# Kernel optimization log

Measured on AMD Instinct MI355X. Metric: run time of the kernel, lower is better.

Reference implementation:

```python
import jax, jax.numpy as jnp
import numpy as np

T1, T2, T3 = 0.05, 0.1, 0.15
EPS = 1e-8  # matches torch cosine_similarity clamp


def _propagate(x, t):
    # GEmbedding: cosine-similarity adjacency  [B,N,F] -> [B,N,N]
    xn = x / jnp.maximum(jnp.linalg.norm(x, axis=-1, keepdims=True), EPS)
    adj = jnp.einsum('bnf,bmf->bnm', xn, xn)
    # F.threshold(adj, t, 0): keep values strictly greater than t
    adj = jnp.where(adj > t, adj, 0.0)
    # GraphAdjNorm: D^{-1/2} A D^{-1/2} via row/col broadcast (same math as
    # the original diag-matmul, without materializing diagonal matrices)
    d = jnp.sum(adj, axis=-1)              # [B,N]
    inv_sqrt = 1.0 / jnp.sqrt(d)           # [B,N]
    adj = adj * inv_sqrt[..., :, None] * inv_sqrt[..., None, :]
    return jnp.einsum('bnm,bmf->bnf', adj, x)


def setup_inputs() -> dict:
    key = jax.random.key(0)
    k1, k2 = jax.random.split(key)
    B, N, F = 8, 2048, 128
    x = jax.random.normal(k1, (B, N, F), dtype=jnp.float32)
    weight = jax.random.normal(k2, (F, F), dtype=jnp.float32) * 0.05
    return {"x": x, "weight": weight}


def reference(x, weight):
    res = x
    h = x
    for t in (T1, T2, T3):
        h = _propagate(h, t)
    h = jax.lax.stop_gradient(h)  # torch.no_grad() block
    return jnp.einsum('bnf,fo->bno', h + res, weight)
```

## Files before the change

kernel.cpp:

```cpp
#include <hip/hip_runtime.h>
#include <hip/hip_bf16.h>
#include <cstdint>

#define BQ 8
#define NQ 2048
#define FQ 128
#define NG (NQ * 16)
#define HSS 256.0f

typedef __attribute__((ext_vector_type(8))) short short8;
typedef __attribute__((ext_vector_type(4))) float f32x4;
typedef __attribute__((ext_vector_type(8))) unsigned short us8;
typedef __attribute__((ext_vector_type(2))) unsigned int u32x2;
typedef __attribute__((ext_vector_type(4))) unsigned int u32x4;

__device__ __forceinline__ unsigned short f2bf(float f) {
    union { float f; unsigned int u; } c; c.f = f;
    unsigned int u = c.u;
    u = (u + 0x7FFFu + ((u >> 16) & 1u)) >> 16;
    return (unsigned short)u;
}
__device__ __forceinline__ float bf2f(unsigned short u) {
    union { unsigned int i; float f; } c; c.i = (unsigned int)u << 16; return c.f;
}
__device__ __forceinline__ unsigned int pk8lo(float a, float b, unsigned int old) {
    return (unsigned int)__builtin_amdgcn_cvt_pk_fp8_f32(a, b, (int)old, false);
}
__device__ __forceinline__ unsigned int pk8hi(float a, float b, unsigned int old) {
    return (unsigned int)__builtin_amdgcn_cvt_pk_fp8_f32(a, b, (int)old, true);
}


__global__ __launch_bounds__(256) void k_rownorm(const float* __restrict__ h,
                                                 unsigned short* __restrict__ xnF,
                                                 const float* __restrict__ W,
                                                 unsigned short* __restrict__ WF) {
    int t = threadIdx.x;
    if (blockIdx.x < 8) {
        int b = blockIdx.x;
        int c2 = t & 15, fc = t >> 4;
        us8 u;
        #pragma unroll
        for (int e = 0; e < 8; ++e)
            u[e] = f2bf(W[(size_t)(fc * 8 + e) * FQ + b * 16 + c2]);
        *(us8*)(WF + b * 2048 + fc * 128 + c2 * 8) = u;
        return;
    }
    int bid = blockIdx.x - 8;
    int rl = t >> 4, j = t & 15;
    size_t row = (size_t)bid * 16 + rl;
    const float* hr = h + row * FQ + j * 8;
    float v[8];
    #pragma unroll
    for (int e = 0; e < 8; ++e) v[e] = hr[e];
    float s = 0.f;
    #pragma unroll
    for (int e = 0; e < 8; ++e) s += v[e] * v[e];
    s += __shfl_xor(s, 1, 64);
    s += __shfl_xor(s, 2, 64);
    s += __shfl_xor(s, 4, 64);
    s += __shfl_xor(s, 8, 64);
    float inv = 1.0f / fmaxf(sqrtf(s), 1e-8f);
    us8 u;
    #pragma unroll
    for (int e = 0; e < 8; ++e) u[e] = f2bf(v[e] * inv);
    *(us8*)(xnF + (size_t)bid * 2048 + j * 128 + rl * 8) = u;
}

__global__ __launch_bounds__(512) void k_adj(const unsigned short* __restrict__ xnF,
                                             unsigned char* __restrict__ adjF,
                                             float* __restrict__ dpart, float t) {
    __shared__ unsigned short As[16384];
    __shared__ union { unsigned short Bsh[16384];
                       unsigned char  T2[128 * 132]; } ub;
    __shared__ float dsm[2][128];
    __shared__ float csm[2][128];

    int bid = blockIdx.x;
    int bb = bid & 7;
    int pr = bid >> 3;
    int I = 0;
    { int p = pr; while (p >= 16 - I) { p -= 16 - I; ++I; } pr = p; }
    int J = I + pr;

    int tid = threadIdx.x;
    int wid = tid >> 6, lane = tid & 63;
    int wr = wid >> 1, wc = wid & 1;
    int g = lane >> 4, c = lane & 15;

    const unsigned short* xb = xnF + (size_t)bb * NQ * FQ;
    int rowb = I * 128 + wr * 32;
    int colb = J * 128 + wc * 64;

    {
        const unsigned short* srcA = xb + (size_t)(I * 8) * 2048;
        const unsigned short* srcB = xb + (size_t)(J * 8) * 2048;
        #pragma unroll
        for (int it = 0; it < 4; ++it) {
            __builtin_amdgcn_global_load_lds(
                (const __attribute__((address_space(1))) void*)(srcA + (size_t)(it * 512 + tid) * 8),
                (__attribute__((address_space(3))) void*)(As + (it * 512 + wid * 64) * 8),
                16, 0, 0);
            __builtin_amdgcn_global_load_lds(
                (const __attribute__((address_space(1))) void*)(srcB + (size_t)(it * 512 + tid) * 8),
                (__attribute__((address_space(3))) void*)(ub.Bsh + (it * 512 + wid * 64) * 8),
                16, 0, 0);
        }
    }
    __syncthreads();

    short8 a[2][4];
    #pragma unroll
    for (int mi = 0; mi < 2; ++mi)
        #pragma unroll
        for (int ks = 0; ks < 4; ++ks)
            a[mi][ks] = *(const short8*)(As + (wr * 2 + mi) * 2048 + (ks * 4 + g) * 128 + c * 8);

    f32x4 acc[2][4];
    #pragma unroll
    for (int mi = 0; mi < 2; ++mi)
        #pragma unroll
        for (int ni = 0; ni < 4; ++ni) acc[mi][ni] = (f32x4){0.f, 0.f, 0.f, 0.f};

    #pragma unroll
    for (int ni = 0; ni < 4; ++ni) {
        short8 b[4];
        #pragma unroll
        for (int ks = 0; ks < 4; ++ks)
            b[ks] = *(const short8*)(ub.Bsh + (wc * 4 + ni) * 2048 + (ks * 4 + g) * 128 + c * 8);
        #pragma unroll
        for (int mi = 0; mi < 2; ++mi)
            #pragma unroll
            for (int ks = 0; ks < 4; ++ks)
                acc[mi][ni] = __builtin_amdgcn_mfma_f32_16x16x32_bf16(a[mi][ks], b[ks], acc[mi][ni], 0, 0, 0);
    }

    __syncthreads();

    unsigned char* adjb = adjF + (size_t)bb * NQ * NQ;
    float dl[2][4];
    float csl[4] = {0.f, 0.f, 0.f, 0.f};
    #pragma unroll
    for (int mi = 0; mi < 2; ++mi)
        #pragma unroll
        for (int r = 0; r < 4; ++r) dl[mi][r] = 0.f;

    #pragma unroll
    for (int mi = 0; mi < 2; ++mi)
        #pragma unroll
        for (int ni = 0; ni < 4; ++ni) {
            f32x4 v = acc[mi][ni];
            float x0 = (v[0] > t) ? v[0] : 0.0f;
            float x1 = (v[1] > t) ? v[1] : 0.0f;
            float x2 = (v[2] > t) ? v[2] : 0.0f;
            float x3 = (v[3] > t) ? v[3] : 0.0f;
            dl[mi][0] += x0; dl[mi][1] += x1; dl[mi][2] += x2; dl[mi][3] += x3;
            csl[ni] += x0 + x1 + x2 + x3;
            unsigned int u = pk8lo(x0, x1, 0u);
            u = pk8hi(x2, x3, u);
            *(unsigned int*)(adjb + (size_t)((colb >> 4) + ni) * NG
                                  + (size_t)((rowb >> 3) + mi * 2 + (g >> 1)) * 128
                                  + c * 8 + (g & 1) * 4) = u;
            if (I != J) {
                int colL = wc * 64 + ni * 16 + c;
                int rowL = wr * 32 + mi * 16 + g * 4;
                *(unsigned int*)(ub.T2 + colL * 132 + rowL) = u;
            }
        }

    #pragma unroll
    for (int mi = 0; mi < 2; ++mi)
        #pragma unroll
        for (int r = 0; r < 4; ++r) {
            float s = dl[mi][r];
            s += __shfl_xor(s, 1, 64);
            s += __shfl_xor(s, 2, 64);
            s += __shfl_xor(s, 4, 64);
            s += __shfl_xor(s, 8, 64);
            dl[mi][r] = s;
        }
    if (c == 0) {
        #pragma unroll
        for (int mi = 0; mi < 2; ++mi)
            #pragma unroll
            for (int r = 0; r < 4; ++r)
                dsm[wc][wr * 32 + mi * 16 + g * 4 + r] = dl[mi][r];
    }
    if (I != J) {
        #pragma unroll
        for (int ni = 0; ni < 4; ++ni) {
            float s = csl[ni];
            s += __shfl_xor(s, 16, 64);
            s += __shfl_xor(s, 32, 64);
            csl[ni] = s;
        }
        if (lane < 16) {
            #pragma unroll
            for (int ni = 0; ni < 4; ++ni)
                csm[wr & 1][wc * 64 + ni * 16 + lane] = csl[ni];
        }
    }
    __syncthreads();
    if (I != J && (wr >= 2) && lane < 16) {
        #pragma unroll
        for (int ni = 0; ni < 4; ++ni)
            csm[wr & 1][wc * 64 + ni * 16 + lane] += csl[ni];
    }
    __syncthreads();

    if (tid < 128)
        dpart[((size_t)J * 8 + bb) * NQ + I * 128 + tid] = dsm[0][tid] + dsm[1][tid];
    if (I != J) {
        if (tid < 128)
            dpart[((size_t)I * 8 + bb) * NQ + J * 128 + tid] = csm[0][tid] + csm[1][tid];
        int ng = wid;
        int mg = lane >> 2;
        int part = lane & 3;
        unsigned int w[8];
        #pragma unroll
        for (int ml = 0; ml < 8; ++ml)
            w[ml] = *(const unsigned int*)(ub.T2 + (mg * 8 + ml) * 132 + ng * 16 + part * 4);
        unsigned int o32[8];
        #pragma unroll
        for (int i = 0; i < 4; ++i)
            #pragma unroll
            for (int h = 0; h < 2; ++h)
                o32[i * 2 + h] = ((w[h * 4 + 0] >> (8 * i)) & 0xFFu)
                               | (((w[h * 4 + 1] >> (8 * i)) & 0xFFu) << 8)
                               | (((w[h * 4 + 2] >> (8 * i)) & 0xFFu) << 16)
                               | (((w[h * 4 + 3] >> (8 * i)) & 0xFFu) << 24);
        unsigned char* dst = adjb + (size_t)(I * 8 + ng) * NG + (size_t)(J * 16 + mg) * 128 + part * 32;
        *(u32x4*)dst        = (u32x4){o32[0], o32[1], o32[2], o32[3]};
        *(u32x4*)(dst + 16) = (u32x4){o32[4], o32[5], o32[6], o32[7]};
    }
}

__global__ __launch_bounds__(256) void k_prep_f32(const float* __restrict__ h,
                                                  const float* __restrict__ dpart,
                                                  float* __restrict__ isq,
                                                  unsigned char* __restrict__ hsF) {
    __shared__ float iv[32];
    int r0 = blockIdx.x * 32;
    int bb = r0 >> 11;
    int m0 = r0 & (NQ - 1);
    int tid = threadIdx.x;
    if (tid < 32) {
        float s = 0.f;
        #pragma unroll
        for (int j = 0; j < 16; ++j)
            s += dpart[((size_t)j * 8 + bb) * NQ + m0 + tid];
        float v = 1.0f / sqrtf(s);
        iv[tid] = v;
        isq[r0 + tid] = v;
    }
    __syncthreads();
    unsigned char* hb = hsF + (size_t)bb * NQ * FQ;
    #pragma unroll
    for (int it = 0; it < 2; ++it) {
        int p = tid + it * 256;
        int f = p & 127, mc = p >> 7;
        float sv[8];
        #pragma unroll
        for (int e = 0; e < 8; ++e)
            sv[e] = h[(size_t)(r0 + mc * 8 + e) * FQ + f] * iv[mc * 8 + e] * HSS;
        u32x2 u;
        u[0] = pk8hi(sv[2], sv[3], pk8lo(sv[0], sv[1], 0u));
        u[1] = pk8hi(sv[6], sv[7], pk8lo(sv[4], sv[5], 0u));
        *(u32x2*)(hb + (size_t)((m0 >> 3) + mc) * 1024 + f * 8) = u;
    }
}

__global__ __launch_bounds__(256) void k_prep_bf16(const unsigned short* __restrict__ h,
                                                   const float* __restrict__ dpart,
                                                   float* __restrict__ isq,
                                                   unsigned char* __restrict__ hsF) {
    __shared__ float iv[32];
    int r0 = blockIdx.x * 32;
    int bb = r0 >> 11;
    int m0 = r0 & (NQ - 1);
    int tid = threadIdx.x;
    if (tid < 32) {
        float s = 0.f;
        #pragma unroll
        for (int j = 0; j < 16; ++j)
            s += dpart[((size_t)j * 8 + bb) * NQ + m0 + tid];
        float v = 1.0f / sqrtf(s);
        iv[tid] = v;
        isq[r0 + tid] = v;
    }
    __syncthreads();
    unsigned char* hb = hsF + (size_t)bb * NQ * FQ;
    #pragma unroll
    for (int it = 0; it < 2; ++it) {
        int p = tid + it * 256;
        int f = p & 127, mc = p >> 7;
        float sv[8];
        #pragma unroll
        for (int e = 0; e < 8; ++e)
            sv[e] = bf2f(h[(size_t)(r0 + mc * 8 + e) * FQ + f]) * iv[mc * 8 + e] * HSS;
        u32x2 u;
        u[0] = pk8hi(sv[2], sv[3], pk8lo(sv[0], sv[1], 0u));
        u[1] = pk8hi(sv[6], sv[7], pk8lo(sv[4], sv[5], 0u));
        *(u32x2*)(hb + (size_t)((m0 >> 3) + mc) * 1024 + f * 8) = u;
    }
}

template<bool LAST>
__global__ __launch_bounds__(512) void k_gemm3(const unsigned char* __restrict__ adjF,
                                               const unsigned char* __restrict__ hsF,
                                               const float* __restrict__ isq,
                                               unsigned short* __restrict__ hout,
                                               unsigned short* __restrict__ xnF,
                                               const unsigned short* __restrict__ WF,
                                               const float* __restrict__ x,
                                               float* __restrict__ out) {
    __shared__ unsigned char BsD[2][32768];
    float (*red)[128] = (float (*)[128])(&BsD[0][0]);

    int bid = blockIdx.x;
    int lb = (bid & 7) * 64 + (bid >> 3);
    int bb = lb >> 6;
    int rt = lb & 63;
    int row0g = rt * 32;
    int tid = threadIdx.x;
    int wid = tid >> 6, lane = tid & 63;
    int g = lane >> 4, c = lane & 15;
    int rg = wid >> 2, kh = wid & 3;
    int wrow = row0g + rg * 16;

    const unsigned char* adjr = adjF + (size_t)bb * NQ * NQ + (size_t)(wrow >> 4) * NG;
    const unsigned char* hb   = hsF + (size_t)bb * NQ * FQ;

    f32x4 acc[8];
    #pragma unroll
    for (int i = 0; i < 8; ++i) acc[i] = (f32x4){0.f, 0.f, 0.f, 0.f};

    int khr = wid >> 1;
    int wlo = wid & 1;

    #define STAGE(P, BUF)                                                           \
        {                                                                           \
            const unsigned char* src_ = hb + (size_t)(khr * 64 + (P) * 8) * 1024 + wlo * 1024; \
            unsigned char* dst_ = (BUF) + khr * 8192 + wlo * 1024;                  \
            _Pragma("unroll")                                                       \
            for (int it_ = 0; it_ < 4; ++it_) {                                     \
                __builtin_amdgcn_global_load_lds(                                   \
                    (const __attribute__((address_space(1))) void*)(src_ + it_ * 2048 + lane * 16), \
                    (__attribute__((address_space(3))) void*)(dst_ + it_ * 2048),   \
                    16, 0, 0);                                                      \
            }                                                                       \
        }

    STAGE(0, BsD[0]);
    __syncthreads();
    for (int ph = 0; ph < 8; ++ph) {
        if (ph < 7) STAGE(ph + 1, BsD[(ph + 1) & 1]);
        const unsigned char* cur = BsD[ph & 1];
        #pragma unroll
        for (int kk2 = 0; kk2 < 2; ++kk2) {
            int mstep = kh * 16 + ph * 2 + kk2;
            long a0 = *(const long*)(adjr + (size_t)(mstep * 4 + g) * 128 + c * 8);
            #pragma unroll
            for (int ct = 0; ct < 8; ++ct) {
                long bfr = *(const long*)(cur + kh * 8192 + kk2 * 4096 + g * 1024 + (ct * 16 + c) * 8);
                acc[ct] = __builtin_amdgcn_mfma_f32_16x16x32_fp8_fp8(a0, bfr, acc[ct], 0, 0, 0);
            }
        }
        __syncthreads();
    }
    #undef STAGE

    #pragma unroll
    for (int s = 0; s < 4; ++s) {
        if (kh == s) {
            #pragma unroll
            for (int ct = 0; ct < 8; ++ct)
                #pragma unroll
                for (int r = 0; r < 4; ++r) {
                    int rl = rg * 16 + g * 4 + r;
                    if (s == 0) red[rl][ct * 16 + c] = acc[ct][r];
                    else        red[rl][ct * 16 + c] += acc[ct][r];
                }
        }
        __syncthreads();
    }

    if constexpr (!LAST) {
        int rl = tid >> 4;
        int j  = tid & 15;
        int n  = row0g + rl;
        float scale = isq[(size_t)bb * NQ + n] * (1.0f / HSS);
        float v[8];
        float s = 0.f;
        #pragma unroll
        for (int e = 0; e < 8; ++e) {
            float xv = red[rl][j * 8 + e] * scale;
            v[e] = xv;
            s += xv * xv;
        }
        s += __shfl_xor(s, 1, 64);
        s += __shfl_xor(s, 2, 64);
        s += __shfl_xor(s, 4, 64);
        s += __shfl_xor(s, 8, 64);
        float inv = 1.0f / fmaxf(sqrtf(s), 1e-8f);

        us8 h0;
        #pragma unroll
        for (int e = 0; e < 8; ++e) h0[e] = f2bf(v[e]);
        *(us8*)(hout + ((size_t)bb * NQ + n) * FQ + j * 8) = h0;

        us8 u0;
        #pragma unroll
        for (int e = 0; e < 8; ++e) u0[e] = f2bf(v[e] * inv);
        unsigned short* xd = xnF + (size_t)bb * NQ * FQ + (size_t)(n >> 4) * 2048
                                 + j * 128 + (n & 15) * 8;
        *(us8*)xd = u0;
    } else {
        unsigned short* hxs = (unsigned short*)(&BsD[1][0]);
        {
            int rl = tid >> 4, j = tid & 15;
            int n = row0g + rl;
            float scale = isq[(size_t)bb * NQ + n] * (1.0f / HSS);
            const float* xr = x + ((size_t)bb * NQ + n) * FQ + j * 8;
            us8 hxv;
            #pragma unroll
            for (int e = 0; e < 8; ++e)
                hxv[e] = f2bf(red[rl][j * 8 + e] * scale + xr[e]);
            int wb = (rl * 256 + j * 16) ^ ((rl & 7) << 4);
            *(us8*)((char*)hxs + wb) = hxv;
        }
        __syncthreads();
        {
            int rg2 = wid >> 2, oq = wid & 3;
            f32x4 oacc[2];
            oacc[0] = (f32x4){0.f, 0.f, 0.f, 0.f};
            oacc[1] = (f32x4){0.f, 0.f, 0.f, 0.f};
            int row = rg2 * 16 + c;
            #pragma unroll
            for (int ks = 0; ks < 4; ++ks) {
                short8 af = *(const short8*)((const char*)hxs
                              + ((row * 256 + ks * 64 + g * 16) ^ ((row & 7) << 4)));
                #pragma unroll
                for (int ct = 0; ct < 2; ++ct) {
                    int og = oq * 2 + ct;
                    short8 bf = *(const short8*)(WF + og * 2048 + (ks * 4 + g) * 128 + c * 8);
                    oacc[ct] = __builtin_amdgcn_mfma_f32_16x16x32_bf16(af, bf, oacc[ct], 0, 0, 0);
                }
            }
            float* ob = out + ((size_t)bb * NQ + row0g) * FQ;
            #pragma unroll
            for (int ct = 0; ct < 2; ++ct)
                #pragma unroll
                for (int r = 0; r < 4; ++r)
                    ob[(size_t)(rg2 * 16 + g * 4 + r) * FQ + oq * 32 + ct * 16 + c] = oacc[ct][r];
        }
    }
}

extern "C" void kernel_launch(void* const* d_in, const int* in_sizes, int n_in,
                              void* d_out, int out_size, void* d_ws, size_t ws_size,
                              hipStream_t stream) {
    const float* x = (const float*)d_in[0];
    const float* W = (const float*)d_in[1];
    float* out = (float*)d_out;
    char* ws = (char*)d_ws;

    const size_t CS   = (size_t)BQ * NQ * FQ;
    const size_t oADJ = 0;
    const size_t oXN  = oADJ + (size_t)BQ * NQ * NQ;
    const size_t oHST = oXN  + CS * 2;
    const size_t oD   = oHST + CS;
    const size_t oISQ = oD   + (size_t)16 * BQ * NQ * 4;
    const size_t oHA  = oISQ + (size_t)BQ * NQ * 4;
    const size_t oHB  = oHA  + CS * 2;
    const size_t oWF  = oHB  + CS * 2;
    const size_t need = oWF  + (size_t)FQ * FQ * 2;
    if (ws_size < need) return;

    unsigned char*  adjF = (unsigned char*)(ws + oADJ);
    unsigned short* xnF  = (unsigned short*)(ws + oXN);
    unsigned char*  hsF  = (unsigned char*)(ws + oHST);
    float* dpart = (float*)(ws + oD);
    float* isq   = (float*)(ws + oISQ);
    unsigned short* hA = (unsigned short*)(ws + oHA);
    unsigned short* hB = (unsigned short*)(ws + oHB);
    unsigned short* WF = (unsigned short*)(ws + oWF);

    const float ts[3] = {0.05f, 0.1f, 0.15f};

    k_rownorm<<<BQ * NQ / 16 + 8, 256, 0, stream>>>(x, xnF, W, WF);
    k_adj<<<BQ * 136, 512, 0, stream>>>(xnF, adjF, dpart, ts[0]);
    k_prep_f32<<<BQ * NQ / 32, 256, 0, stream>>>(x, dpart, isq, hsF);
    k_gemm3<false><<<BQ * 64, 512, 0, stream>>>(adjF, hsF, isq, hA, xnF, WF, x, out);
    k_adj<<<BQ * 136, 512, 0, stream>>>(xnF, adjF, dpart, ts[1]);
    k_prep_bf16<<<BQ * NQ / 32, 256, 0, stream>>>(hA, dpart, isq, hsF);
    k_gemm3<false><<<BQ * 64, 512, 0, stream>>>(adjF, hsF, isq, hB, xnF, WF, x, out);
    k_adj<<<BQ * 136, 512, 0, stream>>>(xnF, adjF, dpart, ts[2]);
    k_prep_bf16<<<BQ * NQ / 32, 256, 0, stream>>>(hB, dpart, isq, hsF);
    k_gemm3<true><<<BQ * 64, 512, 0, stream>>>(adjF, hsF, isq, hA, xnF, WF, x, out);
}
```

Before: 117.1 us.

## Compute transposed adjacency tile with swapped MFMA operands instead of LDS transpose

For off-diagonal tile pairs, the kernel now issues a second MFMA pass with A and B operands swapped, which yields the transposed tile directly in registers. Each wave writes the mirrored fp8 tile and its column sums straight from those registers. This removes the LDS transpose buffer, the byte-shuffling repack and one barrier, and the adjacency is now thresholded and stored per ni step. The cost is twice the MFMA work on off-diagonal tiles and narrower 4-byte scattered global stores for the mirrored tile in place of 16-byte ones.

```diff
diff --git a/kernel.cpp b/kernel.cpp
--- a/kernel.cpp
+++ b/kernel.cpp
@@ -12,7 +12,6 @@
 typedef __attribute__((ext_vector_type(4))) float f32x4;
 typedef __attribute__((ext_vector_type(8))) unsigned short us8;
 typedef __attribute__((ext_vector_type(2))) unsigned int u32x2;
-typedef __attribute__((ext_vector_type(4))) unsigned int u32x4;
 
 __device__ __forceinline__ unsigned short f2bf(float f) {
     union { float f; unsigned int u; } c; c.f = f;
@@ -71,10 +70,9 @@
                                              unsigned char* __restrict__ adjF,
                                              float* __restrict__ dpart, float t) {
     __shared__ unsigned short As[16384];
-    __shared__ union { unsigned short Bsh[16384];
-                       unsigned char  T2[128 * 132]; } ub;
+    __shared__ unsigned short Bsh[16384];
     __shared__ float dsm[2][128];
-    __shared__ float csm[2][128];
+    __shared__ float csm[4][128];
 
     int bid = blockIdx.x;
     int bb = bid & 7;
@@ -103,7 +101,7 @@
                 16, 0, 0);
             __builtin_amdgcn_global_load_lds(
                 (const __attribute__((address_space(1))) void*)(srcB + (size_t)(it * 512 + tid) * 8),
-                (__attribute__((address_space(3))) void*)(ub.Bsh + (it * 512 + wid * 64) * 8),
+                (__attribute__((address_space(3))) void*)(Bsh + (it * 512 + wid * 64) * 8),
                 16, 0, 0);
         }
     }
@@ -116,57 +114,86 @@
         for (int ks = 0; ks < 4; ++ks)
             a[mi][ks] = *(const short8*)(As + (wr * 2 + mi) * 2048 + (ks * 4 + g) * 128 + c * 8);
 
-    f32x4 acc[2][4];
+    unsigned char* adjb = adjF + (size_t)bb * NQ * NQ;
+    float dl[2][4];
     #pragma unroll
     for (int mi = 0; mi < 2; ++mi)
         #pragma unroll
-        for (int ni = 0; ni < 4; ++ni) acc[mi][ni] = (f32x4){0.f, 0.f, 0.f, 0.f};
+        for (int r = 0; r < 4; ++r) dl[mi][r] = 0.f;
 
     #pragma unroll
     for (int ni = 0; ni < 4; ++ni) {
         short8 b[4];
         #pragma unroll
         for (int ks = 0; ks < 4; ++ks)
-            b[ks] = *(const short8*)(ub.Bsh + (wc * 4 + ni) * 2048 + (ks * 4 + g) * 128 + c * 8);
+            b[ks] = *(const short8*)(Bsh + (wc * 4 + ni) * 2048 + (ks * 4 + g) * 128 + c * 8);
+
+        f32x4 accA[2], accB[2];
+        #pragma unroll
+        for (int mi = 0; mi < 2; ++mi) {
+            accA[mi] = (f32x4){0.f, 0.f, 0.f, 0.f};
+            accB[mi] = (f32x4){0.f, 0.f, 0.f, 0.f};
+        }
         #pragma unroll
         for (int mi = 0; mi < 2; ++mi)
             #pragma unroll
             for (int ks = 0; ks < 4; ++ks)
-                acc[mi][ni] = __builtin_amdgcn_mfma_f32_16x16x32_bf16(a[mi][ks], b[ks], acc[mi][ni], 0, 0, 0);
-    }
-
-    __syncthreads();
-
-    unsigned char* adjb = adjF + (size_t)bb * NQ * NQ;
-    float dl[2][4];
-    float csl[4] = {0.f, 0.f, 0.f, 0.f};
-    #pragma unroll
-    for (int mi = 0; mi < 2; ++mi)
-        #pragma unroll
-        for (int r = 0; r < 4; ++r) dl[mi][r] = 0.f;
-
-    #pragma unroll
-    for (int mi = 0; mi < 2; ++mi)
-        #pragma unroll
-        for (int ni = 0; ni < 4; ++ni) {
-            f32x4 v = acc[mi][ni];
+                accA[mi] = __builtin_amdgcn_mfma_f32_16x16x32_bf16(a[mi][ks], b[ks], accA[mi], 0, 0, 0);
+        if (I != J) {
+            #pragma unroll
+            for (int mi = 0; mi < 2; ++mi)
+                #pragma unroll
+                for (int ks = 0; ks < 4; ++ks)
+                    accB[mi] = __builtin_amdgcn_mfma_f32_16x16x32_bf16(b[ks], a[mi][ks], accB[mi], 0, 0, 0);
+        }
+
+        #pragma unroll
+        for (int mi = 0; mi < 2; ++mi) {
+            f32x4 v = accA[mi];
             float x0 = (v[0] > t) ? v[0] : 0.0f;
             float x1 = (v[1] > t) ? v[1] : 0.0f;
             float x2 = (v[2] > t) ? v[2] : 0.0f;
             float x3 = (v[3] > t) ? v[3] : 0.0f;
             dl[mi][0] += x0; dl[mi][1] += x1; dl[mi][2] += x2; dl[mi][3] += x3;
-            csl[ni] += x0 + x1 + x2 + x3;
             unsigned int u = pk8lo(x0, x1, 0u);
             u = pk8hi(x2, x3, u);
             *(unsigned int*)(adjb + (size_t)((colb >> 4) + ni) * NG
                                   + (size_t)((rowb >> 3) + mi * 2 + (g >> 1)) * 128
                                   + c * 8 + (g & 1) * 4) = u;
-            if (I != J) {
-                int colL = wc * 64 + ni * 16 + c;
-                int rowL = wr * 32 + mi * 16 + g * 4;
-                *(unsigned int*)(ub.T2 + colL * 132 + rowL) = u;
+        }
+
+        if (I != J) {
+            float csl[4] = {0.f, 0.f, 0.f, 0.f};
+            #pragma unroll
+            for (int mi = 0; mi < 2; ++mi) {
+                f32x4 v = accB[mi];
+                float y0 = (v[0] > t) ? v[0] : 0.0f;
+                float y1 = (v[1] > t) ? v[1] : 0.0f;
+                float y2 = (v[2] > t) ? v[2] : 0.0f;
+                float y3 = (v[3] > t) ? v[3] : 0.0f;
+                csl[0] += y0; csl[1] += y1; csl[2] += y2; csl[3] += y3;
+                unsigned int u = pk8lo(y0, y1, 0u);
+                u = pk8hi(y2, y3, u);
+                *(unsigned int*)(adjb + (size_t)((rowb >> 4) + mi) * NG
+                                      + (size_t)((colb >> 3) + ni * 2 + (g >> 1)) * 128
+                                      + c * 8 + (g & 1) * 4) = u;
             }
-        }
+            #pragma unroll
+            for (int r = 0; r < 4; ++r) {
+                float s = csl[r];
+                s += __shfl_xor(s, 1, 64);
+                s += __shfl_xor(s, 2, 64);
+                s += __shfl_xor(s, 4, 64);
+                s += __shfl_xor(s, 8, 64);
+                csl[r] = s;
+            }
+            if (c == 0) {
+                #pragma unroll
+                for (int r = 0; r < 4; ++r)
+                    csm[wr][wc * 64 + ni * 16 + g * 4 + r] = csl[r];
+            }
+        }
+    }
 
     #pragma unroll
     for (int mi = 0; mi < 2; ++mi)
@@ -186,53 +213,13 @@
             for (int r = 0; r < 4; ++r)
                 dsm[wc][wr * 32 + mi * 16 + g * 4 + r] = dl[mi][r];
     }
-    if (I != J) {
-        #pragma unroll
-        for (int ni = 0; ni < 4; ++ni) {
-            float s = csl[ni];
-            s += __shfl_xor(s, 16, 64);
-            s += __shfl_xor(s, 32, 64);
-            csl[ni] = s;
-        }
-        if (lane < 16) {
-            #pragma unroll
-            for (int ni = 0; ni < 4; ++ni)
-                csm[wr & 1][wc * 64 + ni * 16 + lane] = csl[ni];
-        }
-    }
-    __syncthreads();
-    if (I != J && (wr >= 2) && lane < 16) {
-        #pragma unroll
-        for (int ni = 0; ni < 4; ++ni)
-            csm[wr & 1][wc * 64 + ni * 16 + lane] += csl[ni];
-    }
     __syncthreads();
 
     if (tid < 128)
         dpart[((size_t)J * 8 + bb) * NQ + I * 128 + tid] = dsm[0][tid] + dsm[1][tid];
-    if (I != J) {
-        if (tid < 128)
-            dpart[((size_t)I * 8 + bb) * NQ + J * 128 + tid] = csm[0][tid] + csm[1][tid];
-        int ng = wid;
-        int mg = lane >> 2;
-        int part = lane & 3;
-        unsigned int w[8];
-        #pragma unroll
-        for (int ml = 0; ml < 8; ++ml)
-            w[ml] = *(const unsigned int*)(ub.T2 + (mg * 8 + ml) * 132 + ng * 16 + part * 4);
-        unsigned int o32[8];
-        #pragma unroll
-        for (int i = 0; i < 4; ++i)
-            #pragma unroll
-            for (int h = 0; h < 2; ++h)
-                o32[i * 2 + h] = ((w[h * 4 + 0] >> (8 * i)) & 0xFFu)
-                               | (((w[h * 4 + 1] >> (8 * i)) & 0xFFu) << 8)
-                               | (((w[h * 4 + 2] >> (8 * i)) & 0xFFu) << 16)
-                               | (((w[h * 4 + 3] >> (8 * i)) & 0xFFu) << 24);
-        unsigned char* dst = adjb + (size_t)(I * 8 + ng) * NG + (size_t)(J * 16 + mg) * 128 + part * 32;
-        *(u32x4*)dst        = (u32x4){o32[0], o32[1], o32[2], o32[3]};
-        *(u32x4*)(dst + 16) = (u32x4){o32[4], o32[5], o32[6], o32[7]};
-    }
+    if (I != J && tid < 128)
+        dpart[((size_t)I * 8 + bb) * NQ + J * 128 + tid] = csm[0][tid] + csm[1][tid]
+                                                         + csm[2][tid] + csm[3][tid];
 }
 
 __global__ __launch_bounds__(256) void k_prep_f32(const float* __restrict__ h,
```

Result: slower. 133.7 us (+14.2%).
